# Performance work log

Measured on AMD Instinct MI355X. Metric: run time of the kernel, lower is better.

The kernel has to match this reference:

```python
import jax, jax.numpy as jnp
import numpy as np

B, S, E, H = 4, 2048, 1024, 16
D = E // H  # per-head dim
SCALE = float(1.0 / np.sqrt(D))


def setup_inputs() -> dict:
    key = jax.random.key(0)
    k1, k2, k3 = jax.random.split(key, 3)
    x = jax.random.normal(k1, (B, S, E), dtype=jnp.float32)
    # xavier_uniform for torch Linear weights (shape [out, in])
    lim_qkv = float(np.sqrt(6.0 / (E + 3 * E)))
    w_qkv = jax.random.uniform(k2, (3 * E, E), minval=-lim_qkv, maxval=lim_qkv, dtype=jnp.float32)
    lim_o = float(np.sqrt(6.0 / (E + E)))
    w_o = jax.random.uniform(k3, (E, E), minval=-lim_o, maxval=lim_o, dtype=jnp.float32)
    return {"x": x, "w_qkv": w_qkv, "w_o": w_o}


def reference(x, w_qkv, w_o):
    b, s, e = x.shape
    # self-attention projection: (b,s,3E) -> (b,s,H,3D) -> chunk into q,k,v
    qkv = (x @ w_qkv.T).reshape(b, s, H, 3 * D)
    q, k, v = jnp.split(qkv, 3, axis=-1)           # each (b,s,H,D)
    q = q.transpose(0, 2, 1, 3)                    # (b,H,s,D)
    k = k.transpose(0, 2, 1, 3)
    v = v.transpose(0, 2, 1, 3)
    logits = jnp.einsum("bhsd,bhtd->bhst", q, k) * SCALE  # (b,H,s,s)
    # NOTE: faithful to source bug — values use raw scaled logits, not softmax(logits)
    values = jnp.einsum("bhst,bhtd->bhsd", logits, v)     # (b,H,s,D)
    values = values.transpose(0, 2, 1, 3).reshape(b, s, e)
    return values @ w_o.T
```

## Files before the change

### kernel.cpp

```cpp
#include <hip/hip_runtime.h>
#include <hip/hip_bf16.h>
#include <cstdint>

#define SCALE_F 0.125f

typedef __attribute__((ext_vector_type(8))) short bf16x8;
typedef __attribute__((ext_vector_type(4))) float f32x4;
typedef __attribute__((ext_vector_type(4))) unsigned short u16x4;
typedef __attribute__((ext_vector_type(8))) unsigned short u16x8;

typedef const __attribute__((address_space(1))) void glb_void;
typedef __attribute__((address_space(3))) void lds_void;

static __device__ __forceinline__ unsigned short f2bf(float f) {
  unsigned u = __builtin_bit_cast(unsigned, f);
  u = (u + 0x7fffu + ((u >> 16) & 1u)) >> 16;
  return (unsigned short)u;
}
static __device__ __forceinline__ float bf2f(unsigned short s) {
  unsigned u = ((unsigned)s) << 16;
  return __builtin_bit_cast(float, u);
}

static __device__ __forceinline__ int xcd_work(int bid, int nwg) {
  int cpx = nwg >> 3;
  return (bid & 7) * cpx + (bid >> 3);
}

__global__ __launch_bounds__(256) void prep(const float* __restrict__ x,
                                            const float* __restrict__ wqkv,
                                            const float* __restrict__ wo,
                                            unsigned short* __restrict__ xb,
                                            unsigned short* __restrict__ xT,
                                            unsigned short* __restrict__ wqt,
                                            unsigned short* __restrict__ wk,
                                            unsigned short* __restrict__ wv,
                                            unsigned short* __restrict__ wob) {
  __shared__ unsigned short lds[64][72];
  const int t = threadIdx.x;
  const int bid = blockIdx.x;

  if (bid < 2048) {
    const int r0 = (bid & 127) * 64, c0 = (bid >> 7) * 64;
#pragma unroll
    for (int pass = 0; pass < 4; ++pass) {
      int r = pass * 16 + (t >> 4);
      int c = (t & 15) * 4;
      float4 v = *(const float4*)(x + (size_t)(r0 + r) * 1024 + c0 + c);
      u16x4 o = { f2bf(v.x), f2bf(v.y), f2bf(v.z), f2bf(v.w) };
      *(u16x4*)(xb + (size_t)(r0 + r) * 1024 + c0 + c) = o;
#pragma unroll
      for (int j = 0; j < 4; ++j) {
        int C = c + j;
        lds[C][r ^ ((C & 7) << 3)] = o[j];
      }
    }
    __syncthreads();
#pragma unroll
    for (int pass = 0; pass < 2; ++pass) {
      int rr = pass * 32 + (t >> 3);
      int cc = (t & 7) * 8;
      u16x8 v = *(const u16x8*)&lds[rr][cc ^ ((rr & 7) << 3)];
      *(u16x8*)(xT + (size_t)(c0 + rr) * 8192 + r0 + cc) = v;
    }
  } else if (bid < 5120) {
    int row = bid - 2048;
    const float* src;
    unsigned short* dst;
    if (row < 1024) {
      int h = row >> 6, k = row & 63;
      src = wqkv + (size_t)(h * 192 + 64 + k) * 1024;
      dst = wk + (size_t)row * 1024;
    } else if (row < 2048) {
      int local = row - 1024;
      int h = local >> 6, k = local & 63;
      src = wqkv + (size_t)(h * 192 + 128 + k) * 1024;
      dst = wv + (size_t)local * 1024;
    } else {
      int local = row - 2048;
      src = wo + (size_t)local * 1024;
      dst = wob + (size_t)local * 1024;
    }
    float4 v = *(const float4*)(src + t * 4);
    u16x4 o = { f2bf(v.x), f2bf(v.y), f2bf(v.z), f2bf(v.w) };
    *(u16x4*)(dst + t * 4) = o;
  } else {
    int tid = bid - 5120;
    const int r0 = (tid & 15) * 64, c0 = (tid >> 4) * 64;
#pragma unroll
    for (int pass = 0; pass < 4; ++pass) {
      int r = pass * 16 + (t >> 4);
      int c = (t & 15) * 4;
      int gr = r0 + r;
      int srcRow = (gr >> 6) * 192 + (gr & 63);
      float4 v = *(const float4*)(wqkv + (size_t)srcRow * 1024 + c0 + c);
      lds[c + 0][r] = f2bf(v.x);
      lds[c + 1][r] = f2bf(v.y);
      lds[c + 2][r] = f2bf(v.z);
      lds[c + 3][r] = f2bf(v.w);
    }
    __syncthreads();
#pragma unroll
    for (int pass = 0; pass < 2; ++pass) {
      int rr = pass * 32 + (t >> 3);
      int cc = (t & 7) * 8;
      *(u16x8*)(wqt + (size_t)(c0 + rr) * 1024 + r0 + cc) = *(const u16x8*)&lds[rr][cc];
    }
  }
}

template<bool F32OUT>
__global__ __launch_bounds__(512) void gemm_bt(const unsigned short* __restrict__ A, int lda,
                                               long aB, long aP,
                                               const unsigned short* __restrict__ Bm, int ldb,
                                               long bB, long bP,
                                               void* __restrict__ Cv, int ldc,
                                               long cB, long cP,
                                               int K, int psplit, int nx, int ny) {
  __shared__ __align__(16) unsigned short Ash[128 * 32];
  __shared__ __align__(16) unsigned short Bsh[128 * 32];
  const int work = xcd_work(blockIdx.x, gridDim.x);
  const int xt = work % nx;
  const int yt = (work / nx) % ny;
  const int z  = work / (nx * ny);
  const int bb = z / psplit, pp = z % psplit;
  A  += (size_t)bb * aB + (size_t)pp * aP;
  Bm += (size_t)bb * bB + (size_t)pp * bP;
  const int t = threadIdx.x;
  const int w = t >> 6, l = t & 63;
  const int lr = l & 15, lk = l >> 4;
  const int m0 = yt * 128, n0 = xt * 128;
  const int wr = (w >> 2) * 64, wc = (w & 3) * 32;
  const int srow = t >> 2, skc = (t & 3) << 3;
  f32x4 acc[4][2] = {};

  for (int k0 = 0; k0 < K; k0 += 32) {
    __builtin_amdgcn_global_load_lds(
        (glb_void*)(A + (size_t)(m0 + srow) * lda + k0 + skc),
        (lds_void*)(Ash + w * 512), 16, 0, 0);
    __builtin_amdgcn_global_load_lds(
        (glb_void*)(Bm + (size_t)(n0 + srow) * ldb + k0 + skc),
        (lds_void*)(Bsh + w * 512), 16, 0, 0);
    __syncthreads();

    bf16x8 af[4], bfv[2];
#pragma unroll
    for (int mi = 0; mi < 4; ++mi)
      af[mi] = *(const bf16x8*)(Ash + (wr + mi * 16 + lr) * 32 + lk * 8);
#pragma unroll
    for (int ni = 0; ni < 2; ++ni)
      bfv[ni] = *(const bf16x8*)(Bsh + (wc + ni * 16 + lr) * 32 + lk * 8);
#pragma unroll
    for (int mi = 0; mi < 4; ++mi)
#pragma unroll
      for (int ni = 0; ni < 2; ++ni)
        acc[mi][ni] = __builtin_amdgcn_mfma_f32_16x16x32_bf16(af[mi], bfv[ni], acc[mi][ni], 0, 0, 0);
    __syncthreads();
  }

#pragma unroll
  for (int mi = 0; mi < 4; ++mi)
#pragma unroll
    for (int ni = 0; ni < 2; ++ni)
#pragma unroll
      for (int r = 0; r < 4; ++r) {
        const size_t row = (size_t)(m0 + wr + mi * 16 + lk * 4 + r);
        const size_t col = (size_t)(n0 + wc + ni * 16 + lr);
        if constexpr (F32OUT)
          ((float*)Cv)[(size_t)bb * cB + (size_t)pp * cP + row * ldc + col] = acc[mi][ni][r];
        else
          ((unsigned short*)Cv)[(size_t)bb * cB + (size_t)pp * cP + row * ldc + col] = f2bf(acc[mi][ni][r]);
      }
}

__global__ __launch_bounds__(512) void gemm_tri(const unsigned short* __restrict__ xT,
                                                unsigned short* __restrict__ Gp) {
  __shared__ __align__(16) unsigned short Ash[128 * 32];
  __shared__ __align__(16) unsigned short Bsh[128 * 32];
  const int work = xcd_work(blockIdx.x, gridDim.x);
  int ti = work % 36;
  const int z = work / 36;
  int mt = 0, accum = 0;
  while (accum + mt + 1 <= ti) { accum += mt + 1; ++mt; }
  int nt = ti - accum;
  const int b = z >> 2, p = z & 3;
  const unsigned short* base = xT + (size_t)b * 2048 + (size_t)p * 512;

  const int t = threadIdx.x;
  const int w = t >> 6, l = t & 63;
  const int lr = l & 15, lk = l >> 4;
  const int m0 = mt * 128, n0 = nt * 128;
  const int wr = (w >> 2) * 64, wc = (w & 3) * 32;
  const int srow = t >> 2, skc = (t & 3) << 3;
  f32x4 acc[4][2] = {};

  for (int k0 = 0; k0 < 512; k0 += 32) {
    __builtin_amdgcn_global_load_lds(
        (glb_void*)(base + (size_t)(m0 + srow) * 8192 + k0 + skc),
        (lds_void*)(Ash + w * 512), 16, 0, 0);
    __builtin_amdgcn_global_load_lds(
        (glb_void*)(base + (size_t)(n0 + srow) * 8192 + k0 + skc),
        (lds_void*)(Bsh + w * 512), 16, 0, 0);
    __syncthreads();

    bf16x8 af[4], bfv[2];
#pragma unroll
    for (int mi = 0; mi < 4; ++mi)
      af[mi] = *(const bf16x8*)(Ash + (wr + mi * 16 + lr) * 32 + lk * 8);
#pragma unroll
    for (int ni = 0; ni < 2; ++ni)
      bfv[ni] = *(const bf16x8*)(Bsh + (wc + ni * 16 + lr) * 32 + lk * 8);
#pragma unroll
    for (int mi = 0; mi < 4; ++mi)
#pragma unroll
      for (int ni = 0; ni < 2; ++ni)
        acc[mi][ni] = __builtin_amdgcn_mfma_f32_16x16x32_bf16(af[mi], bfv[ni], acc[mi][ni], 0, 0, 0);
    __syncthreads();
  }

  unsigned short* out = Gp + (size_t)z * 1048576;
#pragma unroll
  for (int mi = 0; mi < 4; ++mi)
#pragma unroll
    for (int ni = 0; ni < 2; ++ni)
#pragma unroll
      for (int r = 0; r < 4; ++r)
        out[(size_t)(m0 + wr + mi * 16 + lk * 4 + r) * 1024 + n0 + wc + ni * 16 + lr]
            = f2bf(acc[mi][ni][r]);
}

__global__ __launch_bounds__(256) void mirror_reduce(const unsigned short* __restrict__ Gp,
                                                     unsigned short* __restrict__ G) {
  __shared__ unsigned short ldsT[128][128];
  int ti = blockIdx.x;
  int mt = 0, accum = 0;
  while (accum + mt + 1 <= ti) { accum += mt + 1; ++mt; }
  int nt = ti - accum;
  const int b = blockIdx.y;
  const int m0 = mt * 128, n0 = nt * 128;
  const unsigned short* base = Gp + (size_t)b * 4 * 1048576;
  unsigned short* Gb = G + (size_t)b * 1048576;
  const int t = threadIdx.x;

#pragma unroll
  for (int pass = 0; pass < 8; ++pass) {
    int idx = pass * 2048 + t * 8;
    int r = idx >> 7, c = idx & 127;
    float s[8] = {};
#pragma unroll
    for (int p = 0; p < 4; ++p) {
      u16x8 v = *(const u16x8*)(base + (size_t)p * 1048576 + (size_t)(m0 + r) * 1024 + n0 + c);
#pragma unroll
      for (int j = 0; j < 8; ++j) s[j] += bf2f(v[j]);
    }
    u16x8 o;
#pragma unroll
    for (int j = 0; j < 8; ++j) o[j] = f2bf(s[j]);
    *(u16x8*)(Gb + (size_t)(m0 + r) * 1024 + n0 + c) = o;
#pragma unroll
    for (int j = 0; j < 8; ++j) {
      int col = c + j;
      ldsT[col][r ^ (((col >> 3) & 7) << 3)] = o[j];
    }
  }

  if (mt != nt) {
    __syncthreads();
#pragma unroll
    for (int pass = 0; pass < 8; ++pass) {
      int idx = pass * 2048 + t * 8;
      int rr = idx >> 7, cc = idx & 127;
      u16x8 v = *(const u16x8*)&ldsT[rr][cc ^ (((rr >> 3) & 7) << 3)];
      *(u16x8*)(Gb + (size_t)(n0 + rr) * 1024 + m0 + cc) = v;
    }
  }
}

__global__ __launch_bounds__(256) void mt_partial(const unsigned short* __restrict__ T1p,
                                                  const unsigned short* __restrict__ wv,
                                                  float* __restrict__ Mp) {
  __shared__ float Msh[4096];
  const int t = threadIdx.x;
  const int w = t >> 6, l = t & 63;
  const int lr = l & 15, lk = l >> 4;
  const int bh = blockIdx.x, ep = blockIdx.y;
  const int b = bh >> 4, h = bh & 15;
  const int p = w >> 1, half = w & 1;

  for (int i = t; i < 4096; i += 256) Msh[i] = 0.f;
  __syncthreads();

  const unsigned short* Ab = T1p + (size_t)(b * 2 + p) * 1048576 + (size_t)(h * 64) * 1024;
  const unsigned short* Bb = wv + (size_t)(h * 64) * 1024;
  f32x4 acc[4][4] = {};
  const int ebeg = ep * 256 + half * 128;
#pragma unroll
  for (int e0 = ebeg; e0 < ebeg + 128; e0 += 32) {
    bf16x8 af[4], bfv[4];
#pragma unroll
    for (int mi = 0; mi < 4; ++mi)
      af[mi] = *(const bf16x8*)(Ab + (size_t)(mi * 16 + lr) * 1024 + e0 + lk * 8);
#pragma unroll
    for (int ni = 0; ni < 4; ++ni)
      bfv[ni] = *(const bf16x8*)(Bb + (size_t)(ni * 16 + lr) * 1024 + e0 + lk * 8);
#pragma unroll
    for (int mi = 0; mi < 4; ++mi)
#pragma unroll
      for (int ni = 0; ni < 4; ++ni)
        acc[mi][ni] = __builtin_amdgcn_mfma_f32_16x16x32_bf16(af[mi], bfv[ni], acc[mi][ni], 0, 0, 0);
  }
#pragma unroll
  for (int mi = 0; mi < 4; ++mi)
#pragma unroll
    for (int ni = 0; ni < 4; ++ni)
#pragma unroll
      for (int r = 0; r < 4; ++r)
        atomicAdd(&Msh[(mi * 16 + lk * 4 + r) * 64 + ni * 16 + lr], acc[mi][ni][r]);
  __syncthreads();

  float* out = Mp + ((size_t)bh * 4 + ep) * 4096;
  for (int i = t * 4; i < 4096; i += 1024)
    *(float4*)(out + i) = *(const float4*)&Msh[i];
}

__global__ __launch_bounds__(256) void amat_fused(const float* __restrict__ Mp,
                                                  const unsigned short* __restrict__ wqt,
                                                  unsigned short* __restrict__ Amat) {
  __shared__ float Msh[64 * 68];
  __shared__ unsigned short MtSh[64][80];
  const int t = threadIdx.x;
  const int et = blockIdx.x, bh = blockIdx.y;
  const int b = bh >> 4, h = bh & 15;

  const float* base = Mp + (size_t)bh * 16384;
  for (int i = t * 4; i < 4096; i += 1024) {
    float4 s = *(const float4*)(base + i);
#pragma unroll
    for (int p = 1; p < 4; ++p) {
      float4 v = *(const float4*)(base + p * 4096 + i);
      s.x += v.x; s.y += v.y; s.z += v.z; s.w += v.w;
    }
    int k = i >> 6, dp = i & 63;
    *(float4*)&Msh[k * 68 + dp] = s;
  }
  __syncthreads();

  for (int i = t; i < 4096; i += 256) {
    int dp = i >> 6, k = i & 63;
    MtSh[dp][k] = f2bf(Msh[k * 68 + dp] * SCALE_F);
  }
  __syncthreads();

  const int w = t >> 6, l = t & 63;
  const int lr = l & 15, lk = l >> 4;
  const int e0 = et * 128 + w * 32;

  f32x4 acc[2][4] = {};
#pragma unroll
  for (int ks = 0; ks < 2; ++ks) {
    bf16x8 af[2], bfv[4];
#pragma unroll
    for (int mi = 0; mi < 2; ++mi)
      af[mi] = *(const bf16x8*)(wqt + (size_t)(e0 + mi * 16 + lr) * 1024 + h * 64 + ks * 32 + lk * 8);
#pragma unroll
    for (int ni = 0; ni < 4; ++ni)
      bfv[ni] = *(const bf16x8*)(&MtSh[ni * 16 + lr][ks * 32 + lk * 8]);
#pragma unroll
    for (int mi = 0; mi < 2; ++mi)
#pragma unroll
      for (int ni = 0; ni < 4; ++ni)
        acc[mi][ni] = __builtin_amdgcn_mfma_f32_16x16x32_bf16(af[mi], bfv[ni], acc[mi][ni], 0, 0, 0);
  }
#pragma unroll
  for (int mi = 0; mi < 2; ++mi)
#pragma unroll
    for (int ni = 0; ni < 4; ++ni)
#pragma unroll
      for (int r = 0; r < 4; ++r)
        Amat[(size_t)b * 1048576 + (size_t)(e0 + mi * 16 + lk * 4 + r) * 1024 + h * 64 + ni * 16 + lr]
            = f2bf(acc[mi][ni][r]);
}

extern "C" void kernel_launch(void* const* d_in, const int* in_sizes, int n_in,
                              void* d_out, int out_size, void* d_ws, size_t ws_size,
                              hipStream_t stream) {
  const float* x    = (const float*)d_in[0];
  const float* wqkv = (const float*)d_in[1];
  const float* wo   = (const float*)d_in[2];
  float* out = (float*)d_out;

  char* ws = (char*)d_ws;
  const size_t MB = 1048576;
  unsigned short* xb   = (unsigned short*)(ws + 0);
  unsigned short* xT   = (unsigned short*)(ws + 16 * MB);
  unsigned short* wqt  = (unsigned short*)(ws + 32 * MB);
  unsigned short* wk   = (unsigned short*)(ws + 34 * MB);
  unsigned short* wv   = (unsigned short*)(ws + 36 * MB);
  unsigned short* wob  = (unsigned short*)(ws + 38 * MB);
  unsigned short* Gp   = (unsigned short*)(ws + 40 * MB);
  unsigned short* G    = (unsigned short*)(ws + 72 * MB);
  unsigned short* T1p  = (unsigned short*)(ws + 40 * MB);
  float*          Mp   = (float*)        (ws + 56 * MB);
  unsigned short* Amat = (unsigned short*)(ws + 61 * MB);
  unsigned short* Weff = (unsigned short*)(ws + 40 * MB);

  const long M1 = 1048576;

  prep<<<5376, 256, 0, stream>>>(x, wqkv, wo, xb, xT, wqt, wk, wv, wob);

  gemm_tri<<<576, 512, 0, stream>>>(xT, Gp);
  mirror_reduce<<<dim3(36, 4), 256, 0, stream>>>(Gp, G);

  gemm_bt<false><<<512, 512, 0, stream>>>(wk, 1024, 0, 512,
                                          G, 1024, M1, 512,
                                          (void*)T1p, 1024, 2 * M1, M1, 512, 2, 8, 8);

  mt_partial<<<dim3(64, 4), 256, 0, stream>>>(T1p, wv, Mp);

  amat_fused<<<dim3(8, 64), 256, 0, stream>>>(Mp, wqt, Amat);

  gemm_bt<false><<<256, 512, 0, stream>>>(wob, 1024, 0, 0,
                                          Amat, 1024, M1, 0,
                                          (void*)Weff, 1024, M1, 0, 1024, 1, 8, 8);

  gemm_bt<true><<<512, 512, 0, stream>>>(xb, 1024, 2048 * 1024L, 0,
                                         Weff, 1024, M1, 0,
                                         (void*)out, 1024, 2048 * 1024L, 0, 1024, 1, 8, 16);
}
```

Measured before the change: 151.4 us.

## Double-buffer LDS tiles and XOR-swizzle layout in GEMM kernels

Both GEMM kernels now keep two LDS buffers and issue the global-to-LDS loads for the next K slice before computing on the current one, so memory latency can overlap with MFMA work. The global source column is XOR-swizzled by row and the fragment reads apply the matching XOR, which is meant to cut LDS bank conflicts. This doubles LDS use per block, which may reduce occupancy. The loop-end barrier is the only one left, so correctness depends on it covering both the buffer reuse and the wait for the prefetched loads.

```diff
diff --git a/kernel.cpp b/kernel.cpp
--- a/kernel.cpp
+++ b/kernel.cpp
@@ -117,8 +117,8 @@
                                                void* __restrict__ Cv, int ldc,
                                                long cB, long cP,
                                                int K, int psplit, int nx, int ny) {
-  __shared__ __align__(16) unsigned short Ash[128 * 32];
-  __shared__ __align__(16) unsigned short Bsh[128 * 32];
+  __shared__ __align__(16) unsigned short Ash[2][128 * 32];
+  __shared__ __align__(16) unsigned short Bsh[2][128 * 32];
   const int work = xcd_work(blockIdx.x, gridDim.x);
   const int xt = work % nx;
   const int yt = (work / nx) % ny;
@@ -131,25 +131,32 @@
   const int lr = l & 15, lk = l >> 4;
   const int m0 = yt * 128, n0 = xt * 128;
   const int wr = (w >> 2) * 64, wc = (w & 3) * 32;
-  const int srow = t >> 2, skc = (t & 3) << 3;
+  const int srow = t >> 2;
+  const int skc = ((t & 3) ^ ((srow >> 1) & 3)) << 3;
+  const size_t aOff = (size_t)(m0 + srow) * lda + skc;
+  const size_t bOff = (size_t)(n0 + srow) * ldb + skc;
+  const int fxor = ((lk ^ ((lr >> 1) & 3)) << 3);
   f32x4 acc[4][2] = {};
 
-  for (int k0 = 0; k0 < K; k0 += 32) {
-    __builtin_amdgcn_global_load_lds(
-        (glb_void*)(A + (size_t)(m0 + srow) * lda + k0 + skc),
-        (lds_void*)(Ash + w * 512), 16, 0, 0);
-    __builtin_amdgcn_global_load_lds(
-        (glb_void*)(Bm + (size_t)(n0 + srow) * ldb + k0 + skc),
-        (lds_void*)(Bsh + w * 512), 16, 0, 0);
-    __syncthreads();
-
+  __builtin_amdgcn_global_load_lds((glb_void*)(A + aOff), (lds_void*)(Ash[0] + w * 512), 16, 0, 0);
+  __builtin_amdgcn_global_load_lds((glb_void*)(Bm + bOff), (lds_void*)(Bsh[0] + w * 512), 16, 0, 0);
+  __syncthreads();
+
+  int cur = 0;
+  for (int k0 = 0; k0 < K; k0 += 32, cur ^= 1) {
+    if (k0 + 32 < K) {
+      __builtin_amdgcn_global_load_lds((glb_void*)(A + aOff + k0 + 32),
+                                       (lds_void*)(Ash[cur ^ 1] + w * 512), 16, 0, 0);
+      __builtin_amdgcn_global_load_lds((glb_void*)(Bm + bOff + k0 + 32),
+                                       (lds_void*)(Bsh[cur ^ 1] + w * 512), 16, 0, 0);
+    }
     bf16x8 af[4], bfv[2];
 #pragma unroll
     for (int mi = 0; mi < 4; ++mi)
-      af[mi] = *(const bf16x8*)(Ash + (wr + mi * 16 + lr) * 32 + lk * 8);
+      af[mi] = *(const bf16x8*)(Ash[cur] + (wr + mi * 16 + lr) * 32 + fxor);
 #pragma unroll
     for (int ni = 0; ni < 2; ++ni)
-      bfv[ni] = *(const bf16x8*)(Bsh + (wc + ni * 16 + lr) * 32 + lk * 8);
+      bfv[ni] = *(const bf16x8*)(Bsh[cur] + (wc + ni * 16 + lr) * 32 + fxor);
 #pragma unroll
     for (int mi = 0; mi < 4; ++mi)
 #pragma unroll
@@ -175,8 +182,8 @@
 
 __global__ __launch_bounds__(512) void gemm_tri(const unsigned short* __restrict__ xT,
                                                 unsigned short* __restrict__ Gp) {
-  __shared__ __align__(16) unsigned short Ash[128 * 32];
-  __shared__ __align__(16) unsigned short Bsh[128 * 32];
+  __shared__ __align__(16) unsigned short Ash[2][128 * 32];
+  __shared__ __align__(16) unsigned short Bsh[2][128 * 32];
   const int work = xcd_work(blockIdx.x, gridDim.x);
   int ti = work % 36;
   const int z = work / 36;
@@ -191,25 +198,32 @@
   const int lr = l & 15, lk = l >> 4;
   const int m0 = mt * 128, n0 = nt * 128;
   const int wr = (w >> 2) * 64, wc = (w & 3) * 32;
-  const int srow = t >> 2, skc = (t & 3) << 3;
+  const int srow = t >> 2;
+  const int skc = ((t & 3) ^ ((srow >> 1) & 3)) << 3;
+  const size_t aOff = (size_t)(m0 + srow) * 8192 + skc;
+  const size_t bOff = (size_t)(n0 + srow) * 8192 + skc;
+  const int fxor = ((lk ^ ((lr >> 1) & 3)) << 3);
   f32x4 acc[4][2] = {};
 
-  for (int k0 = 0; k0 < 512; k0 += 32) {
-    __builtin_amdgcn_global_load_lds(
-        (glb_void*)(base + (size_t)(m0 + srow) * 8192 + k0 + skc),
-        (lds_void*)(Ash + w * 512), 16, 0, 0);
-    __builtin_amdgcn_global_load_lds(
-        (glb_void*)(base + (size_t)(n0 + srow) * 8192 + k0 + skc),
-        (lds_void*)(Bsh + w * 512), 16, 0, 0);
-    __syncthreads();
-
+  __builtin_amdgcn_global_load_lds((glb_void*)(base + aOff), (lds_void*)(Ash[0] + w * 512), 16, 0, 0);
+  __builtin_amdgcn_global_load_lds((glb_void*)(base + bOff), (lds_void*)(Bsh[0] + w * 512), 16, 0, 0);
+  __syncthreads();
+
+  int cur = 0;
+  for (int k0 = 0; k0 < 512; k0 += 32, cur ^= 1) {
+    if (k0 + 32 < 512) {
+      __builtin_amdgcn_global_load_lds((glb_void*)(base + aOff + k0 + 32),
+                                       (lds_void*)(Ash[cur ^ 1] + w * 512), 16, 0, 0);
+      __builtin_amdgcn_global_load_lds((glb_void*)(base + bOff + k0 + 32),
+                                       (lds_void*)(Bsh[cur ^ 1] + w * 512), 16, 0, 0);
+    }
     bf16x8 af[4], bfv[2];
 #pragma unroll
     for (int mi = 0; mi < 4; ++mi)
-      af[mi] = *(const bf16x8*)(Ash + (wr + mi * 16 + lr) * 32 + lk * 8);
+      af[mi] = *(const bf16x8*)(Ash[cur] + (wr + mi * 16 + lr) * 32 + fxor);
 #pragma unroll
     for (int ni = 0; ni < 2; ++ni)
-      bfv[ni] = *(const bf16x8*)(Bsh + (wc + ni * 16 + lr) * 32 + lk * 8);
+      bfv[ni] = *(const bf16x8*)(Bsh[cur] + (wc + ni * 16 + lr) * 32 + fxor);
 #pragma unroll
     for (int mi = 0; mi < 4; ++mi)
 #pragma unroll
```

Result: faster. 145.1 us (-4.1%).
